# Kernel optimization log

Measured on AMD Instinct MI355X. Metric: run time of the kernel, lower is better.

The kernel has to match this reference:

```python
import jax, jax.numpy as jnp
import numpy as np
import math

B, N, M = 128, 16, 32
D_OBS, D_OUT = 128, 128            # obs_input_dim, obs_output_dim (== obs_output_dim_other)
D_OA, D_AV = 136, 128              # obs_act_input_dim, obs_act_output_dim
D_OBS_O, D_OA_O, D_AV_O = 128, 136, 128
D_FINAL_IN, D_HID, D_FINAL_OUT = 256, 64, 1
N_ACT = 8


def setup_inputs() -> dict:
    key = jax.random.key(0)
    ks = jax.random.split(key, 16)
    s = 0.05
    return {
        "states": jax.random.normal(ks[0], (B, N, D_OBS), jnp.float32),
        "policies": jax.random.uniform(ks[1], (B, N, N_ACT), jnp.float32),
        "actions": jax.random.uniform(ks[2], (B, N, N_ACT), jnp.float32),
        "states_other": jax.random.normal(ks[3], (B, M, D_OBS_O), jnp.float32),
        "actions_other": jax.random.uniform(ks[4], (B, M, N_ACT), jnp.float32),
        # weights stored as [in, out] (torch Linear applies x @ W.T)
        "Wk": jax.random.normal(ks[5], (D_OBS, D_OUT), jnp.float32) * s,
        "Wq": jax.random.normal(ks[6], (D_OBS, D_OUT), jnp.float32) * s,
        "Wv": jax.random.normal(ks[7], (D_OA, D_AV), jnp.float32) * s,
        "Wk_o": jax.random.normal(ks[8], (D_OBS_O, D_OUT), jnp.float32) * s,
        "Wq_o": jax.random.normal(ks[9], (D_OBS, D_OUT), jnp.float32) * s,
        "Wv_o": jax.random.normal(ks[10], (D_OA_O, D_AV_O), jnp.float32) * s,
        "W1": jax.random.normal(ks[11], (D_FINAL_IN, D_HID), jnp.float32) * s,
        "W2": jax.random.normal(ks[12], (D_HID, D_FINAL_OUT), jnp.float32) * s,
    }


def reference(states, policies, actions, states_other, actions_other,
              Wk, Wq, Wv, Wk_o, Wq_o, Wv_o, W1, W2):
    d_k = float(D_OUT)
    d_k_o = float(D_OUT)  # d_k_obs_other = obs_output_dim_other

    obs_actions = jnp.concatenate([states, actions], axis=-1)   # [B,N,D_OA]
    obs_policy = jnp.concatenate([states, policies], axis=-1)   # [B,N,D_OA]

    k = states @ Wk                                             # [B,N,D_OUT]
    q = states @ Wq
    score = jnp.einsum('bid,bjd->bij', q, k)                    # [B,N,N]
    # torch softmaxes over the key axis (after reshape gymnastics)
    weight = jax.nn.softmax(score / math.sqrt(d_k), axis=-1)    # [B,N,N]
    ret_weight = weight

    # oap[b,j,k] = obs_policy[b,k] if j==k else obs_actions[b,k]
    eye = jnp.eye(N, dtype=states.dtype)[None, :, :, None]      # [1,N,N,1]
    oap = eye * obs_policy[:, None, :, :] + (1.0 - eye) * obs_actions[:, None, :, :]  # [B,N,N,D_OA]
    av = jnp.tanh(oap @ Wv)                                     # [B,N(j),N(k),D_AV]

    # torch: repeat av over a new agent axis i, multiply by weight[b,i,k], sum over k
    wav = jnp.einsum('bik,bjkd->bijd', weight, av)              # [B,N,N,D_AV]

    obs_actions_other = jnp.concatenate([states_other, actions_other], axis=-1)  # [B,M,D_OA_O]
    k_o = states_other @ Wk_o                                   # [B,M,D_OUT]
    q_o = states @ Wq_o                                         # [B,N,D_OUT]
    av_o = jnp.tanh(obs_actions_other @ Wv_o)                   # [B,M,D_AV_O]

    score_o = jnp.einsum('bid,bmd->bim', q_o, k_o)              # [B,N,M]
    # torch softmax dim=-2: over the agent axis (faithful, even if unusual)
    weight_o = jax.nn.softmax(score_o / math.sqrt(d_k_o), axis=1)  # [B,N,M]
    wav_o = jnp.einsum('bim,bmd->bid', weight_o, av_o)          # [B,N,D_AV_O]
    wav_o_b = jnp.broadcast_to(wav_o[:, :, None, :], (wav_o.shape[0], N, N, D_AV_O))

    node = jnp.concatenate([wav, wav_o_b], axis=-1)             # [B,N,N,256]
    h = jax.nn.leaky_relu(node @ W1)                            # [B,N,N,64]
    value = h @ W2                                              # [B,N,N,1]
    return value, ret_weight, weight_o[..., None]
```

## Files before the change

### kernel.cpp

```cpp
#include <hip/hip_runtime.h>
#include <math.h>

#define NB 128
#define NN 16
#define MM 32
#define DD 128
#define NACT 8
#define HH 64

#define WS_W  0
#define WS_WO 32768
#define WS_P  98304
#define WS_V  229376
#define WS_PO 360448
#define WS_FLOATS 622592

__device__ float g_ws[WS_FLOATS];

__device__ __forceinline__ float4 tanh4(float4 v) {
    float4 r; r.x = tanhf(v.x); r.y = tanhf(v.y); r.z = tanhf(v.z); r.w = tanhf(v.w); return r;
}
__device__ __forceinline__ void fma4(float4& a, float s, const float4& w) {
    a.x += s * w.x; a.y += s * w.y; a.z += s * w.z; a.w += s * w.w;
}

__launch_bounds__(256, 2)
__global__ void k_main(const float* __restrict__ states,   const float* __restrict__ policies,
                       const float* __restrict__ actions,  const float* __restrict__ states_o,
                       const float* __restrict__ actions_o,
                       const float* __restrict__ Wq,  const float* __restrict__ Wk,
                       const float* __restrict__ Wv,  const float* __restrict__ Wqo,
                       const float* __restrict__ Wko, const float* __restrict__ Wvo,
                       const float* __restrict__ W1,  float* __restrict__ out) {
    __shared__ float sm[13200];
    const int unit = blockIdx.x >> 7;
    const int b = blockIdx.x & 127;
    const int t = threadIdx.x;
    const float scale = 0.08838834764831845f;

    if (unit == 0) {
        float* s_st = sm;
        float* s_q  = sm + 2112;
        float* s_k  = sm + 4224;
        {
            int row = t >> 5, c4 = (t & 31) * 4;
            *(float4*)&s_st[row * 132 + c4] = *(const float4*)(states + b * 2048 + row * 128 + c4);
            int t2 = t + 256, row2 = t2 >> 5, c42 = (t2 & 31) * 4;
            *(float4*)&s_st[row2 * 132 + c42] = *(const float4*)(states + b * 2048 + row2 * 128 + c42);
        }
        __syncthreads();
        {
            const int p = t >> 5, c4 = (t & 31) * 4;
            float4 q0 = {0,0,0,0}, q1 = {0,0,0,0}, k0 = {0,0,0,0}, k1 = {0,0,0,0};
            #pragma unroll 8
            for (int kk = 0; kk < DD; ++kk) {
                float x0 = s_st[(2 * p) * 132 + kk], x1 = s_st[(2 * p + 1) * 132 + kk];
                float4 wq = *(const float4*)(Wq + kk * 128 + c4);
                float4 wk = *(const float4*)(Wk + kk * 128 + c4);
                fma4(q0, x0, wq); fma4(q1, x1, wq);
                fma4(k0, x0, wk); fma4(k1, x1, wk);
            }
            *(float4*)&s_q[(2 * p) * 132 + c4] = q0; *(float4*)&s_q[(2 * p + 1) * 132 + c4] = q1;
            *(float4*)&s_k[(2 * p) * 132 + c4] = k0; *(float4*)&s_k[(2 * p + 1) * 132 + c4] = k1;
        }
        __syncthreads();
        {
            int i = t >> 4, j = t & 15;
            float acc = 0.f;
            #pragma unroll 8
            for (int d = 0; d < DD; ++d) acc += s_q[i * 132 + d] * s_k[j * 132 + d];
            acc *= scale;
            float mx = acc;
            #pragma unroll
            for (int msk = 8; msk >= 1; msk >>= 1) mx = fmaxf(mx, __shfl_xor(mx, msk, 16));
            float e = expf(acc - mx);
            float sum = e;
            #pragma unroll
            for (int msk = 8; msk >= 1; msk >>= 1) sum += __shfl_xor(sum, msk, 16);
            float wv = e / sum;
            out[NB * 256 + b * 256 + t] = wv;
            g_ws[WS_W + b * 256 + t] = wv;
        }
    } else if (unit == 1) {
        float* s_st = sm;
        float* s_aa = sm + 2112;
        float* s_df = sm + 4224;
        float* s_ac = sm + 6336;
        float* s_po = sm + 6464;
        {
            int row = t >> 5, c4 = (t & 31) * 4;
            *(float4*)&s_st[row * 132 + c4] = *(const float4*)(states + b * 2048 + row * 128 + c4);
            int t2 = t + 256, row2 = t2 >> 5, c42 = (t2 & 31) * 4;
            *(float4*)&s_st[row2 * 132 + c42] = *(const float4*)(states + b * 2048 + row2 * 128 + c42);
            if (t < 128) {
                s_ac[t] = actions [b * 128 + t];
                s_po[t] = policies[b * 128 + t];
            }
        }
        __syncthreads();
        {
            const int p = t >> 5, c4 = (t & 31) * 4;
            float4 a0 = {0,0,0,0}, a1 = {0,0,0,0};
            #pragma unroll 8
            for (int kk = 0; kk < DD; ++kk) {
                float4 wv = *(const float4*)(Wv + kk * 128 + c4);
                fma4(a0, s_st[(2 * p) * 132 + kk], wv);
                fma4(a1, s_st[(2 * p + 1) * 132 + kk], wv);
            }
            float4 aa0 = a0, aa1 = a1, ap0 = a0, ap1 = a1;
            #pragma unroll
            for (int k = 0; k < NACT; ++k) {
                float4 wv = *(const float4*)(Wv + (DD + k) * 128 + c4);
                fma4(aa0, s_ac[(2 * p) * 8 + k], wv); fma4(aa1, s_ac[(2 * p + 1) * 8 + k], wv);
                fma4(ap0, s_po[(2 * p) * 8 + k], wv); fma4(ap1, s_po[(2 * p + 1) * 8 + k], wv);
            }
            aa0 = tanh4(aa0); aa1 = tanh4(aa1); ap0 = tanh4(ap0); ap1 = tanh4(ap1);
            float4 d0, d1;
            d0.x = ap0.x - aa0.x; d0.y = ap0.y - aa0.y; d0.z = ap0.z - aa0.z; d0.w = ap0.w - aa0.w;
            d1.x = ap1.x - aa1.x; d1.y = ap1.y - aa1.y; d1.z = ap1.z - aa1.z; d1.w = ap1.w - aa1.w;
            *(float4*)&s_aa[(2 * p) * 132 + c4] = aa0; *(float4*)&s_aa[(2 * p + 1) * 132 + c4] = aa1;
            *(float4*)&s_df[(2 * p) * 132 + c4] = d0;  *(float4*)&s_df[(2 * p + 1) * 132 + c4] = d1;
        }
        __syncthreads();
        {
            const int i = t >> 4, h4 = (t & 15) * 4;
            float4 pa = {0,0,0,0}, va = {0,0,0,0};
            #pragma unroll 8
            for (int kk = 0; kk < DD; ++kk) {
                float4 w4 = *(const float4*)(W1 + kk * HH + h4);
                fma4(pa, s_aa[i * 132 + kk], w4);
                fma4(va, s_df[i * 132 + kk], w4);
            }
            *(float4*)(g_ws + WS_P + b * 1024 + i * 64 + h4) = pa;
            *(float4*)(g_ws + WS_V + b * 1024 + i * 64 + h4) = va;
        }
    } else if (unit == 2) {
        float* s_st  = sm;
        float* s_qo  = sm + 2112;
        float* s_sto = sm + 4224;
        float* s_koT = sm + 8448;
        float* s_wo  = sm + 12672;
        {
            int row = t >> 5, c4 = (t & 31) * 4;
            *(float4*)&s_st[row * 132 + c4] = *(const float4*)(states + b * 2048 + row * 128 + c4);
            int t2 = t + 256, row2 = t2 >> 5, c42 = (t2 & 31) * 4;
            *(float4*)&s_st[row2 * 132 + c42] = *(const float4*)(states + b * 2048 + row2 * 128 + c42);
            #pragma unroll
            for (int u = 0; u < 4; ++u) {
                int f = t + u * 256, r = f >> 5, cc = (f & 31) * 4;
                *(float4*)&s_sto[r * 132 + cc] = *(const float4*)(states_o + b * 4096 + r * 128 + cc);
            }
        }
        __syncthreads();
        {
            const int p = t >> 5, c4 = (t & 31) * 4;
            float4 g0 = {0,0,0,0}, g1 = {0,0,0,0};
            float4 o0 = {0,0,0,0}, o1 = {0,0,0,0}, o2 = {0,0,0,0}, o3 = {0,0,0,0};
            #pragma unroll 8
            for (int kk = 0; kk < DD; ++kk) {
                float4 wq = *(const float4*)(Wqo + kk * 128 + c4);
                float4 wk = *(const float4*)(Wko + kk * 128 + c4);
                fma4(g0, s_st[(2 * p) * 132 + kk], wq);
                fma4(g1, s_st[(2 * p + 1) * 132 + kk], wq);
                fma4(o0, s_sto[(4 * p) * 132 + kk], wk);
                fma4(o1, s_sto[(4 * p + 1) * 132 + kk], wk);
                fma4(o2, s_sto[(4 * p + 2) * 132 + kk], wk);
                fma4(o3, s_sto[(4 * p + 3) * 132 + kk], wk);
            }
            *(float4*)&s_qo[(2 * p) * 132 + c4] = g0;
            *(float4*)&s_qo[(2 * p + 1) * 132 + c4] = g1;
            s_koT[(c4+0)*33 + 4*p]   = o0.x; s_koT[(c4+1)*33 + 4*p]   = o0.y; s_koT[(c4+2)*33 + 4*p]   = o0.z; s_koT[(c4+3)*33 + 4*p]   = o0.w;
            s_koT[(c4+0)*33 + 4*p+1] = o1.x; s_koT[(c4+1)*33 + 4*p+1] = o1.y; s_koT[(c4+2)*33 + 4*p+1] = o1.z; s_koT[(c4+3)*33 + 4*p+1] = o1.w;
            s_koT[(c4+0)*33 + 4*p+2] = o2.x; s_koT[(c4+1)*33 + 4*p+2] = o2.y; s_koT[(c4+2)*33 + 4*p+2] = o2.z; s_koT[(c4+3)*33 + 4*p+2] = o2.w;
            s_koT[(c4+0)*33 + 4*p+3] = o3.x; s_koT[(c4+1)*33 + 4*p+3] = o3.y; s_koT[(c4+2)*33 + 4*p+3] = o3.z; s_koT[(c4+3)*33 + 4*p+3] = o3.w;
        }
        __syncthreads();
        {
            int i = t >> 5, m = t & 31;
            float a0 = 0.f, a1 = 0.f;
            #pragma unroll 8
            for (int d = 0; d < DD; ++d) {
                float kv = s_koT[d * 33 + m];
                a0 += s_qo[i * 132 + d] * kv;
                a1 += s_qo[(i + 8) * 132 + d] * kv;
            }
            s_wo[i * 33 + m] = a0 * scale;
            s_wo[(i + 8) * 33 + m] = a1 * scale;
        }
        __syncthreads();
        {
            int m = t >> 4, i = t & 15;
            float x = s_wo[i * 33 + m];
            float mx = x;
            #pragma unroll
            for (int msk = 8; msk >= 1; msk >>= 1) mx = fmaxf(mx, __shfl_xor(mx, msk, 16));
            float e = expf(x - mx);
            float sum = e;
            #pragma unroll
            for (int msk = 8; msk >= 1; msk >>= 1) sum += __shfl_xor(sum, msk, 16);
            float wv = e / sum;
            out[2 * NB * 256 + b * 512 + i * 32 + m] = wv;
            g_ws[WS_WO + b * 512 + i * 32 + m] = wv;
            int m2 = 16 + (t >> 4), i2 = t & 15;
            float x2 = s_wo[i2 * 33 + m2];
            float mx2 = x2;
            #pragma unroll
            for (int msk = 8; msk >= 1; msk >>= 1) mx2 = fmaxf(mx2, __shfl_xor(mx2, msk, 16));
            float e2 = expf(x2 - mx2);
            float sum2 = e2;
            #pragma unroll
            for (int msk = 8; msk >= 1; msk >>= 1) sum2 += __shfl_xor(sum2, msk, 16);
            float wv2 = e2 / sum2;
            out[2 * NB * 256 + b * 512 + i2 * 32 + m2] = wv2;
            g_ws[WS_WO + b * 512 + i2 * 32 + m2] = wv2;
        }
    } else {
        float* s_sto = sm;
        float* s_avo = sm + 4224;
        float* s_ao  = sm + 8448;
        {
            #pragma unroll
            for (int u = 0; u < 4; ++u) {
                int f = t + u * 256, r = f >> 5, cc = (f & 31) * 4;
                *(float4*)&s_sto[r * 132 + cc] = *(const float4*)(states_o + b * 4096 + r * 128 + cc);
            }
            s_ao[t] = actions_o[b * 256 + t];
        }
        __syncthreads();
        {
            const int p = t >> 5, c4 = (t & 31) * 4;
            float4 v0 = {0,0,0,0}, v1 = {0,0,0,0}, v2 = {0,0,0,0}, v3 = {0,0,0,0};
            #pragma unroll 8
            for (int kk = 0; kk < DD; ++kk) {
                float4 wv = *(const float4*)(Wvo + kk * 128 + c4);
                fma4(v0, s_sto[(4 * p) * 132 + kk], wv);
                fma4(v1, s_sto[(4 * p + 1) * 132 + kk], wv);
                fma4(v2, s_sto[(4 * p + 2) * 132 + kk], wv);
                fma4(v3, s_sto[(4 * p + 3) * 132 + kk], wv);
            }
            #pragma unroll
            for (int k = 0; k < NACT; ++k) {
                float4 wv = *(const float4*)(Wvo + (DD + k) * 128 + c4);
                fma4(v0, s_ao[(4 * p) * 8 + k], wv);
                fma4(v1, s_ao[(4 * p + 1) * 8 + k], wv);
                fma4(v2, s_ao[(4 * p + 2) * 8 + k], wv);
                fma4(v3, s_ao[(4 * p + 3) * 8 + k], wv);
            }
            *(float4*)&s_avo[(4 * p) * 132 + c4]     = tanh4(v0);
            *(float4*)&s_avo[(4 * p + 1) * 132 + c4] = tanh4(v1);
            *(float4*)&s_avo[(4 * p + 2) * 132 + c4] = tanh4(v2);
            *(float4*)&s_avo[(4 * p + 3) * 132 + c4] = tanh4(v3);
        }
        __syncthreads();
        {
            const int r = t >> 4, h4 = (t & 15) * 4;
            float4 p0 = {0,0,0,0}, p1 = {0,0,0,0};
            #pragma unroll 8
            for (int kk = 0; kk < DD; ++kk) {
                float4 w4 = *(const float4*)(W1 + (DD + kk) * HH + h4);
                fma4(p0, s_avo[r * 132 + kk], w4);
                fma4(p1, s_avo[(r + 16) * 132 + kk], w4);
            }
            *(float4*)(g_ws + WS_PO + b * 2048 + r * 64 + h4) = p0;
            *(float4*)(g_ws + WS_PO + b * 2048 + (r + 16) * 64 + h4) = p1;
        }
    }
}

__launch_bounds__(256, 2)
__global__ void k_fin(const float* __restrict__ W2, float* __restrict__ out) {
    __shared__ float s_w [16 * 17];
    __shared__ float s_wo[16 * 33];
    __shared__ float s_P [16 * 64];
    __shared__ float s_Po[32 * 64];
    __shared__ float s_V [16 * 68];
    __shared__ float s_U [16 * 68];
    __shared__ float s_W2[HH];
    const int b = blockIdx.x, t = threadIdx.x;

    s_w[(t >> 4) * 17 + (t & 15)] = g_ws[WS_W + b * 256 + t];
    s_wo[(t >> 5) * 33 + (t & 31)] = g_ws[WS_WO + b * 512 + t];
    s_wo[((t + 256) >> 5) * 33 + (t & 31)] = g_ws[WS_WO + b * 512 + 256 + t];
    ((float4*)s_P)[t] = ((const float4*)(g_ws + WS_P + b * 1024))[t];
    ((float4*)s_Po)[t] = ((const float4*)(g_ws + WS_PO + b * 2048))[t];
    ((float4*)s_Po)[t + 256] = ((const float4*)(g_ws + WS_PO + b * 2048))[t + 256];
    #pragma unroll
    for (int u = 0; u < 4; ++u) {
        int idx = t + u * 256;
        s_V[(idx >> 6) * 68 + (idx & 63)] = g_ws[WS_V + b * 1024 + idx];
    }
    if (t < HH) s_W2[t] = W2[t];
    __syncthreads();

    {
        int i = t >> 4, h4 = (t & 15) * 4;
        float4 u = {0,0,0,0};
        #pragma unroll
        for (int k = 0; k < NN; ++k) fma4(u, s_w[i * 17 + k], *(const float4*)&s_P[k * 64 + h4]);
        #pragma unroll
        for (int m = 0; m < MM; ++m) fma4(u, s_wo[i * 33 + m], *(const float4*)&s_Po[m * 64 + h4]);
        *(float4*)&s_U[i * 68 + h4] = u;
    }
    __syncthreads();

    {
        int i = t >> 4, j = t & 15;
        float wij = s_w[i * 17 + j];
        float acc = 0.f;
        #pragma unroll
        for (int h = 0; h < HH; ++h) {
            float x = s_U[i * 68 + h] + wij * s_V[j * 68 + h];
            x = (x > 0.f) ? x : 0.01f * x;
            acc += x * s_W2[h];
        }
        out[b * 256 + t] = acc;
    }
}

extern "C" void kernel_launch(void* const* d_in, const int* in_sizes, int n_in,
                              void* d_out, int out_size, void* d_ws, size_t ws_size,
                              hipStream_t stream) {
    const float* states    = (const float*)d_in[0];
    const float* policies  = (const float*)d_in[1];
    const float* actions   = (const float*)d_in[2];
    const float* states_o  = (const float*)d_in[3];
    const float* actions_o = (const float*)d_in[4];
    const float* Wk        = (const float*)d_in[5];
    const float* Wq        = (const float*)d_in[6];
    const float* Wv        = (const float*)d_in[7];
    const float* Wk_o      = (const float*)d_in[8];
    const float* Wq_o      = (const float*)d_in[9];
    const float* Wv_o      = (const float*)d_in[10];
    const float* W1        = (const float*)d_in[11];
    const float* W2        = (const float*)d_in[12];
    float* out = (float*)d_out;

    hipLaunchKernelGGL(k_main, dim3(512), dim3(256), 0, stream,
                       states, policies, actions, states_o, actions_o,
                       Wq, Wk, Wv, Wq_o, Wk_o, Wv_o, W1, out);
    hipLaunchKernelGGL(k_fin, dim3(128), dim3(256), 0, stream, W2, out);
}
```

Before: 104.4 us.

## Fuse final stage into main kernel via per-batch atomic last-block counter

```diff
diff --git a/kernel.cpp b/kernel.cpp
--- a/kernel.cpp
+++ b/kernel.cpp
@@ -16,6 +16,7 @@
 #define WS_FLOATS 622592
 
 __device__ float g_ws[WS_FLOATS];
+__device__ unsigned g_ctr[NB];
 
 __device__ __forceinline__ float4 tanh4(float4 v) {
     float4 r; r.x = tanhf(v.x); r.y = tanhf(v.y); r.z = tanhf(v.z); r.w = tanhf(v.w); return r;
@@ -31,8 +32,10 @@
                        const float* __restrict__ Wq,  const float* __restrict__ Wk,
                        const float* __restrict__ Wv,  const float* __restrict__ Wqo,
                        const float* __restrict__ Wko, const float* __restrict__ Wvo,
-                       const float* __restrict__ W1,  float* __restrict__ out) {
+                       const float* __restrict__ W1,  const float* __restrict__ W2,
+                       float* __restrict__ out) {
     __shared__ float sm[13200];
+    __shared__ int s_last;
     const int unit = blockIdx.x >> 7;
     const int b = blockIdx.x & 127;
     const int t = threadIdx.x;
@@ -265,53 +268,60 @@
             *(float4*)(g_ws + WS_PO + b * 2048 + (r + 16) * 64 + h4) = p1;
         }
     }
-}
-
-__launch_bounds__(256, 2)
-__global__ void k_fin(const float* __restrict__ W2, float* __restrict__ out) {
-    __shared__ float s_w [16 * 17];
-    __shared__ float s_wo[16 * 33];
-    __shared__ float s_P [16 * 64];
-    __shared__ float s_Po[32 * 64];
-    __shared__ float s_V [16 * 68];
-    __shared__ float s_U [16 * 68];
-    __shared__ float s_W2[HH];
-    const int b = blockIdx.x, t = threadIdx.x;
-
-    s_w[(t >> 4) * 17 + (t & 15)] = g_ws[WS_W + b * 256 + t];
-    s_wo[(t >> 5) * 33 + (t & 31)] = g_ws[WS_WO + b * 512 + t];
-    s_wo[((t + 256) >> 5) * 33 + (t & 31)] = g_ws[WS_WO + b * 512 + 256 + t];
-    ((float4*)s_P)[t] = ((const float4*)(g_ws + WS_P + b * 1024))[t];
-    ((float4*)s_Po)[t] = ((const float4*)(g_ws + WS_PO + b * 2048))[t];
-    ((float4*)s_Po)[t + 256] = ((const float4*)(g_ws + WS_PO + b * 2048))[t + 256];
+
+    __threadfence();
+    __syncthreads();
+    if (t == 0) {
+        unsigned old = atomicAdd(&g_ctr[b], 1u);
+        s_last = (old == 3u);
+        if (s_last) g_ctr[b] = 0;
+    }
+    __syncthreads();
+    if (!s_last) return;
+    __threadfence();
+
+    float* e_w  = sm;
+    float* e_wo = sm + 272;
+    float* e_P  = sm + 800;
+    float* e_Po = sm + 1824;
+    float* e_V  = sm + 3872;
+    float* e_U  = sm + 4960;
+    float* e_W2 = sm + 6048;
+
+    e_w[(t >> 4) * 17 + (t & 15)] = g_ws[WS_W + b * 256 + t];
+    e_wo[(t >> 5) * 33 + (t & 31)] = g_ws[WS_WO + b * 512 + t];
+    e_wo[((t + 256) >> 5) * 33 + (t & 31)] = g_ws[WS_WO + b * 512 + 256 + t];
+    ((float4*)e_P)[t] = ((const float4*)(g_ws + WS_P + b * 1024))[t];
+    ((float4*)e_Po)[t] = ((const float4*)(g_ws + WS_PO + b * 2048))[t];
+    ((float4*)e_Po)[t + 256] = ((const float4*)(g_ws + WS_PO + b * 2048))[t + 256];
     #pragma unroll
     for (int u = 0; u < 4; ++u) {
         int idx = t + u * 256;
-        s_V[(idx >> 6) * 68 + (idx & 63)] = g_ws[WS_V + b * 1024 + idx];
-    }
-    if (t < HH) s_W2[t] = W2[t];
+        e_V[(idx >> 6) * 68 + (idx & 63)] = g_ws[WS_V + b * 1024 + idx];
+    }
+    if (t < HH) e_W2[t] = W2[t];
     __syncthreads();
 
     {
         int i = t >> 4, h4 = (t & 15) * 4;
         float4 u = {0,0,0,0};
         #pragma unroll
-        for (int k = 0; k < NN; ++k) fma4(u, s_w[i * 17 + k], *(const float4*)&s_P[k * 64 + h4]);
+        for (int k = 0; k < NN; ++k) fma4(u, e_w[i * 17 + k], *(const float4*)&e_P[k * 64 + h4]);
         #pragma unroll
-        for (int m = 0; m < MM; ++m) fma4(u, s_wo[i * 33 + m], *(const float4*)&s_Po[m * 64 + h4]);
-        *(float4*)&s_U[i * 68 + h4] = u;
+        for (int m = 0; m < MM; ++m) fma4(u, e_wo[i * 33 + m], *(const float4*)&e_Po[m * 64 + h4]);
+        *(float4*)&e_U[i * 68 + h4] = u;
     }
     __syncthreads();
 
     {
         int i = t >> 4, j = t & 15;
-        float wij = s_w[i * 17 + j];
+        float wij = e_w[i * 17 + j];
         float acc = 0.f;
         #pragma unroll
         for (int h = 0; h < HH; ++h) {
-            float x = s_U[i * 68 + h] + wij * s_V[j * 68 + h];
+            float x = e_U[i * 68 + h] + wij * e_V[j * 68 + h];
             x = (x > 0.f) ? x : 0.01f * x;
-            acc += x * s_W2[h];
+            acc += x * e_W2[h];
         }
         out[b * 256 + t] = acc;
     }
@@ -337,6 +347,5 @@
 
     hipLaunchKernelGGL(k_main, dim3(512), dim3(256), 0, stream,
                        states, policies, actions, states_o, actions_o,
-                       Wq, Wk, Wv, Wq_o, Wk_o, Wv_o, W1, out);
-    hipLaunchKernelGGL(k_fin, dim3(128), dim3(256), 0, stream, W2, out);
+                       Wq, Wk, Wv, Wq_o, Wk_o, Wv_o, W1, W2, out);
 }
```

Result: slower. 158.5 us (+51.8%).
